# Performance work log

Hardware: AMD Instinct MI355X
Metric: run time of the kernel (lower is better)

Reference implementation:

```python
import jax, jax.numpy as jnp
import numpy as np

N_NODES = 50000
N_EDGES = 400000
N_GRAPHS = 256
NUM_TYPES = 200
EMB = 64
HID = 128
HEADS = 4
GDIM = 256  # graph_embed_dim
NUM_CLASSES = 20
EPS = 1e-5
NEG_SLOPE = 0.2


def _gat_conv(h, src, dst, W, a_src, a_dst, bias, heads, out_c, concat):
    """PyG GATConv (with self-loops already appended to src/dst)."""
    n = h.shape[0]
    x = (h @ W.T).reshape(n, heads, out_c)                       # [N,H,C]
    al_s = jnp.einsum('nhc,hc->nh', x, a_src)                    # [N,H]
    al_d = jnp.einsum('nhc,hc->nh', x, a_dst)
    e = jax.nn.leaky_relu(al_s[src] + al_d[dst], NEG_SLOPE)      # [E',H]
    # segment softmax over destination node
    e_max = jax.ops.segment_max(e, dst, num_segments=n)
    e_exp = jnp.exp(e - e_max[dst])
    denom = jax.ops.segment_sum(e_exp, dst, num_segments=n)
    alpha = e_exp / denom[dst]                                   # [E',H]
    out = jax.ops.segment_sum(alpha[:, :, None] * x[src], dst, num_segments=n)  # [N,H,C]
    out = out.reshape(n, heads * out_c) if concat else out.mean(axis=1)
    return out + bias


def _batchnorm(h, gamma, beta):
    # training-mode BatchNorm1d over node dim (biased variance, as torch)
    m = h.mean(axis=0)
    v = jnp.mean((h - m) ** 2, axis=0)
    return (h - m) * jax.lax.rsqrt(v + EPS) * gamma + beta


def setup_inputs() -> dict:
    key = jax.random.key(0)
    ks = jax.random.split(key, 32)
    s = 0.1
    inp = {
        'x': jax.random.randint(ks[0], (N_NODES,), 0, NUM_TYPES),
        'edge_index': jax.random.randint(ks[1], (2, N_EDGES), 0, N_NODES),
        'depth': jax.random.uniform(ks[2], (N_NODES,), jnp.float32),
        'batch': jnp.sort(jax.random.randint(ks[3], (N_NODES,), 0, N_GRAPHS)),
        'emb_table': jax.random.normal(ks[4], (NUM_TYPES, EMB), jnp.float32) * s,
        'depth_w': jax.random.normal(ks[5], (EMB, 1), jnp.float32) * s,
        'depth_b': jnp.zeros((EMB,), jnp.float32),
        'W0': jax.random.normal(ks[6], (HEADS * HID, EMB), jnp.float32) * s,
        'as0': jax.random.normal(ks[7], (HEADS, HID), jnp.float32) * s,
        'ad0': jax.random.normal(ks[8], (HEADS, HID), jnp.float32) * s,
        'b0': jnp.zeros((HEADS * HID,), jnp.float32),
        'g0': jnp.ones((HEADS * HID,), jnp.float32),
        'be0': jnp.zeros((HEADS * HID,), jnp.float32),
        'W1': jax.random.normal(ks[9], (HEADS * HID, HEADS * HID), jnp.float32) * s,
        'as1': jax.random.normal(ks[10], (HEADS, HID), jnp.float32) * s,
        'ad1': jax.random.normal(ks[11], (HEADS, HID), jnp.float32) * s,
        'b1': jnp.zeros((HEADS * HID,), jnp.float32),
        'g1': jnp.ones((HEADS * HID,), jnp.float32),
        'be1': jnp.zeros((HEADS * HID,), jnp.float32),
        # layer 2: 512 -> 128, 1 head, no concat
        'W2': jax.random.normal(ks[12], (GDIM // 2, HEADS * HID), jnp.float32) * s,
        'as2': jax.random.normal(ks[13], (1, GDIM // 2), jnp.float32) * s,
        'ad2': jax.random.normal(ks[14], (1, GDIM // 2), jnp.float32) * s,
        'b2': jnp.zeros((GDIM // 2,), jnp.float32),
        'g2': jnp.ones((GDIM // 2,), jnp.float32),
        'be2': jnp.zeros((GDIM // 2,), jnp.float32),
        # classifier: 256 -> 256 -> 20
        'cw1': jax.random.normal(ks[15], (GDIM, 2 * (GDIM // 2)), jnp.float32) * s,
        'cb1': jnp.zeros((GDIM,), jnp.float32),
        'cw2': jax.random.normal(ks[16], (NUM_CLASSES, GDIM), jnp.float32) * s,
        'cb2': jnp.zeros((NUM_CLASSES,), jnp.float32),
    }
    return inp


def reference(x, edge_index, depth, batch, emb_table, depth_w, depth_b,
              W0, as0, ad0, b0, g0, be0,
              W1, as1, ad1, b1, g1, be1,
              W2, as2, ad2, b2, g2, be2,
              cw1, cb1, cw2, cb2):
    n = x.shape[0]
    # node features: type embedding + depth projection
    h = emb_table[x] + (depth[:, None] @ depth_w.T + depth_b)    # [N,64]
    # add self-loops once (PyG GATConv default add_self_loops=True)
    loop = jnp.arange(n)
    src = jnp.concatenate([edge_index[0], loop])
    dst = jnp.concatenate([edge_index[1], loop])
    layers = [
        (W0, as0, ad0, b0, g0, be0, HEADS, HID, True),
        (W1, as1, ad1, b1, g1, be1, HEADS, HID, True),
        (W2, as2, ad2, b2, g2, be2, 1, GDIM // 2, False),
    ]
    for (W, a_s, a_d, b, g, be, heads, out_c, concat) in layers:
        h = _gat_conv(h, src, dst, W, a_s, a_d, b, heads, out_c, concat)
        h = _batchnorm(h, g, be)
        h = jax.nn.elu(h)
        # dropout: eval mode -> identity
    # global mean / max pooling per graph
    ones = jnp.ones((n,), h.dtype)
    counts = jax.ops.segment_sum(ones, batch, num_segments=N_GRAPHS)
    h_mean = jax.ops.segment_sum(h, batch, num_segments=N_GRAPHS) / jnp.maximum(counts, 1.0)[:, None]
    h_max = jax.ops.segment_max(h, batch, num_segments=N_GRAPHS)
    emb = jnp.concatenate([h_mean, h_max], axis=-1)              # [G,256]
    # classifier (dropout off in eval)
    hidden = jax.nn.relu(emb @ cw1.T + cb1)
    return hidden @ cw2.T + cb2                                  # [G,20]
```

## Files before the change

kernel.cpp:

```cpp
#include <hip/hip_runtime.h>
#include <hip/hip_bf16.h>

#define N_NODES 50000
#define N_PAD 50048
#define NBY 391
#define N_EDGES 400000
#define EP (N_EDGES + N_NODES)
#define N_GRAPHS 256
#define EMB 64
#define HID 128
#define HEADS 4
#define GDIM 256
#define NUM_CLASSES 20
#define EPS_BN 1e-5f
#define NEG_SLOPE 0.2f
#define NB_AGG 2048

typedef __attribute__((ext_vector_type(8))) short short8;
typedef __attribute__((ext_vector_type(4))) float f32x4;
typedef _Float16 h8 __attribute__((ext_vector_type(8)));
typedef _Float16 h2 __attribute__((ext_vector_type(2)));

#define GLD(g, l)                                                              \
    __builtin_amdgcn_global_load_lds(                                          \
        (const __attribute__((address_space(1))) void*)(g),                    \
        (__attribute__((address_space(3))) void*)(l), 16, 0, 0)

__device__ __forceinline__ unsigned short f2b(float x) {
    union { float f; unsigned u; } a; a.f = x;
    unsigned r = a.u + 0x7FFF + ((a.u >> 16) & 1);
    return (unsigned short)(r >> 16);
}
__device__ __forceinline__ float b2f(unsigned short h) {
    union { unsigned u; float f; } a; a.u = (unsigned)h << 16;
    return a.f;
}

__global__ void k_node_init(const int* __restrict__ x, const float* __restrict__ depth,
                            const float* __restrict__ emb_table, const float* __restrict__ dw,
                            const float* __restrict__ db, float* __restrict__ h) {
    int i = blockIdx.x * blockDim.x + threadIdx.x;
    if (i >= N_NODES * EMB) return;
    int n = i >> 6, c = i & 63;
    h[i] = emb_table[x[n] * EMB + c] + depth[n] * dw[c] + db[c];
}

__global__ void k_deg(const int* __restrict__ ei, int* __restrict__ deg) {
    int e = blockIdx.x * blockDim.x + threadIdx.x;
    if (e >= EP) return;
    int dst = (e < N_EDGES) ? ei[N_EDGES + e] : (e - N_EDGES);
    atomicAdd(&deg[dst], 1);
}

__global__ void k_scanA(const int* __restrict__ deg, int* __restrict__ incl, int* __restrict__ bsums) {
    __shared__ int sh[1024];
    int t = threadIdx.x;
    int i = blockIdx.x * 1024 + t;
    int v = (i < N_NODES) ? deg[i] : 0;
    int xv = v;
    sh[t] = xv;
    __syncthreads();
    for (int off = 1; off < 1024; off <<= 1) {
        int y = (t >= off) ? sh[t - off] : 0;
        __syncthreads();
        xv += y;
        sh[t] = xv;
        __syncthreads();
    }
    if (i < N_NODES) incl[i] = xv;
    if (t == 1023) bsums[blockIdx.x] = xv;
}

__global__ void k_scanC(const int* __restrict__ incl, const int* __restrict__ deg,
                        const int* __restrict__ bsums, int* __restrict__ offs) {
    int i = blockIdx.x * blockDim.x + threadIdx.x;
    int b = i >> 10;
    int add = 0;
    for (int k = 0; k < b; k++) add += bsums[k];
    if (i < N_NODES) offs[i] = incl[i] - deg[i] + add;
    if (i == 0) offs[N_NODES] = EP;
}

__global__ void k_scatter(const int* __restrict__ ei, const int* __restrict__ offs,
                          int* __restrict__ cnt, int* __restrict__ csr) {
    int e = blockIdx.x * blockDim.x + threadIdx.x;
    if (e >= EP) return;
    int src, dst;
    if (e < N_EDGES) { src = ei[e]; dst = ei[N_EDGES + e]; }
    else { src = e - N_EDGES; dst = src; }
    int pos = atomicAdd(&cnt[dst], 1);
    csr[offs[dst] + pos] = src;
}

__device__ __forceinline__ void split1(const float* __restrict__ in, unsigned short* __restrict__ hi,
                                       unsigned short* __restrict__ lo, int i) {
    int f = i * 4;
    float4 v = *(const float4*)(in + f);
    ushort4 h, l;
    h.x = f2b(v.x); l.x = f2b(v.x - b2f(h.x));
    h.y = f2b(v.y); l.y = f2b(v.y - b2f(h.y));
    h.z = f2b(v.z); l.z = f2b(v.z - b2f(h.z));
    h.w = f2b(v.w); l.w = f2b(v.w - b2f(h.w));
    *(ushort4*)(hi + f) = h;
    *(ushort4*)(lo + f) = l;
}

__global__ __launch_bounds__(256) void k_setup(const float* __restrict__ W0, const float* __restrict__ as0,
                                               const float* __restrict__ ad0, const float* __restrict__ W1,
                                               const float* __restrict__ W2,
                                               unsigned short* __restrict__ W0h, unsigned short* __restrict__ W0l,
                                               unsigned short* __restrict__ W1h, unsigned short* __restrict__ W1l,
                                               unsigned short* __restrict__ W2h, unsigned short* __restrict__ W2l,
                                               float* __restrict__ wtil,
                                               float* __restrict__ bn0, float* __restrict__ bn1,
                                               float* __restrict__ bn2) {
    int b = blockIdx.x, t = threadIdx.x;
    if (b < 256) {
        split1(W1, W1h, W1l, b * 256 + t);
    } else if (b < 288) {
        split1(W0, W0h, W0l, (b - 256) * 256 + t);
    } else if (b < 352) {
        split1(W2, W2h, W2l, (b - 288) * 256 + t);
    } else if (b == 352) {
        int h = t >> 6, k = t & 63;
        float ss = 0.f, sd = 0.f;
        for (int c = 0; c < 128; c++) {
            float w = W0[(size_t)(h * 128 + c) * 64 + k];
            ss += w * as0[h * 128 + c];
            sd += w * ad0[h * 128 + c];
        }
        wtil[t] = ss;
        wtil[256 + t] = sd;
    } else {
        for (int i = t; i < 1024; i += 256) { bn0[i] = 0.f; bn1[i] = 0.f; bn2[i] = 0.f; }
    }
}

__global__ __launch_bounds__(256) void k_bnsplit(unsigned short* __restrict__ hi,
                                                 unsigned short* __restrict__ lo,
                                                 const float* __restrict__ sums,
                                                 const float* __restrict__ gamma,
                                                 const float* __restrict__ beta,
                                                 int M, int total4) {
    int i = blockIdx.x * blockDim.x + threadIdx.x;
    if (i >= total4) return;
    int f = i * 4;
    int c = f & (M - 1);
    float4 s4 = *(const float4*)(sums + c);
    float4 q4 = *(const float4*)(sums + M + c);
    float4 g4 = *(const float4*)(gamma + c);
    float4 be4 = *(const float4*)(beta + c);
    const float invN = 1.f / (float)N_NODES;
    float4 sc, sh;
    {
        float m = s4.x * invN; float var = q4.x * invN - m * m;
        sc.x = g4.x * __frsqrt_rn(var + EPS_BN); sh.x = be4.x - m * sc.x;
        m = s4.y * invN; var = q4.y * invN - m * m;
        sc.y = g4.y * __frsqrt_rn(var + EPS_BN); sh.y = be4.y - m * sc.y;
        m = s4.z * invN; var = q4.z * invN - m * m;
        sc.z = g4.z * __frsqrt_rn(var + EPS_BN); sh.z = be4.z - m * sc.z;
        m = s4.w * invN; var = q4.w * invN - m * m;
        sc.w = g4.w * __frsqrt_rn(var + EPS_BN); sh.w = be4.w - m * sc.w;
    }
    ushort4 h4 = *(const ushort4*)(hi + f);
    ushort4 l4 = *(const ushort4*)(lo + f);
    float4 v;
    v.x = b2f(h4.x) + b2f(l4.x);
    v.y = b2f(h4.y) + b2f(l4.y);
    v.z = b2f(h4.z) + b2f(l4.z);
    v.w = b2f(h4.w) + b2f(l4.w);
    float x;
    x = v.x * sc.x + sh.x; v.x = x > 0.f ? x : expm1f(x);
    x = v.y * sc.y + sh.y; v.y = x > 0.f ? x : expm1f(x);
    x = v.z * sc.z + sh.z; v.z = x > 0.f ? x : expm1f(x);
    x = v.w * sc.w + sh.w; v.w = x > 0.f ? x : expm1f(x);
    ushort4 h, l;
    h.x = f2b(v.x); l.x = f2b(v.x - b2f(h.x));
    h.y = f2b(v.y); l.y = f2b(v.y - b2f(h.y));
    h.z = f2b(v.z); l.z = f2b(v.z - b2f(h.z));
    h.w = f2b(v.w); l.w = f2b(v.w - b2f(h.w));
    *(ushort4*)(hi + f) = h;
    *(ushort4*)(lo + f) = l;
}

__global__ __launch_bounds__(256) void k_al0(const float* __restrict__ h0,
                                             const float* __restrict__ wtil,
                                             float* __restrict__ als, float* __restrict__ ald) {
    int wid = threadIdx.x >> 6, lane = threadIdx.x & 63;
    int n = blockIdx.x * 4 + wid;
    if (n >= N_NODES) return;
    float v = h0[(size_t)n * 64 + lane];
#pragma unroll
    for (int h = 0; h < 4; h++) {
        float ps = v * wtil[h * 64 + lane];
        float pd = v * wtil[256 + h * 64 + lane];
        for (int off = 32; off; off >>= 1) {
            ps += __shfl_xor(ps, off);
            pd += __shfl_xor(pd, off);
        }
        if (lane == 0) { als[n * 4 + h] = ps; ald[n * 4 + h] = pd; }
    }
}

__global__ __launch_bounds__(256) void k_agg0(const float* __restrict__ h0,
                                              const float* __restrict__ als,
                                              const float* __restrict__ ald_g,
                                              const int* __restrict__ offs,
                                              const int* __restrict__ csr,
                                              unsigned short* __restrict__ outh,
                                              unsigned short* __restrict__ outl) {
    const int lane = threadIdx.x & 63;
    const int wwid = threadIdx.x >> 6;
    const int q = lane >> 4, l = lane & 15;
    const int gw = blockIdx.x * 4 + wwid;
    const int stride = gridDim.x * 16;
    for (int n = gw * 4 + q; n < N_NODES; n += stride) {
        int s0 = offs[n], s1 = offs[n + 1];
        float aldl = (l < 4) ? ald_g[n * 4 + l] : 0.f;
        float acc[4][4] = {};
        float den[4] = {};
        int e = s0;
        for (; e + 2 <= s1; e += 2) {
            int srcA = csr[e], srcB = csr[e + 1];
            float wA = 0.f, wB = 0.f;
            if (l < 4) {
                float a1 = als[srcA * 4 + l] + aldl;
                a1 = a1 > 0.f ? a1 : NEG_SLOPE * a1;
                wA = expf(a1);
                float a2 = als[srcB * 4 + l] + aldl;
                a2 = a2 > 0.f ? a2 : NEG_SLOPE * a2;
                wB = expf(a2);
            }
            float4 vA = *(const float4*)(h0 + (size_t)srcA * 64 + l * 4);
            float4 vB = *(const float4*)(h0 + (size_t)srcB * 64 + l * 4);
#pragma unroll
            for (int h = 0; h < 4; h++) {
                float whA = __shfl(wA, q * 16 + h);
                float whB = __shfl(wB, q * 16 + h);
                den[h] += whA + whB;
                acc[h][0] += whA * vA.x + whB * vB.x;
                acc[h][1] += whA * vA.y + whB * vB.y;
                acc[h][2] += whA * vA.z + whB * vB.z;
                acc[h][3] += whA * vA.w + whB * vB.w;
            }
        }
        for (; e < s1; e++) {
            int src = csr[e];
            float w = 0.f;
            if (l < 4) {
                float a1 = als[src * 4 + l] + aldl;
                a1 = a1 > 0.f ? a1 : NEG_SLOPE * a1;
                w = expf(a1);
            }
            float4 v = *(const float4*)(h0 + (size_t)src * 64 + l * 4);
#pragma unroll
            for (int h = 0; h < 4; h++) {
                float wh = __shfl(w, q * 16 + h);
                den[h] += wh;
                acc[h][0] += wh * v.x;
                acc[h][1] += wh * v.y;
                acc[h][2] += wh * v.z;
                acc[h][3] += wh * v.w;
            }
        }
#pragma unroll
        for (int h = 0; h < 4; h++) {
            float id = 1.f / den[h];
            float o0 = acc[h][0] * id, o1 = acc[h][1] * id;
            float o2 = acc[h][2] * id, o3 = acc[h][3] * id;
            ushort4 hh, ll;
            hh.x = f2b(o0); ll.x = f2b(o0 - b2f(hh.x));
            hh.y = f2b(o1); ll.y = f2b(o1 - b2f(hh.y));
            hh.z = f2b(o2); ll.z = f2b(o2 - b2f(hh.z));
            hh.w = f2b(o3); ll.w = f2b(o3 - b2f(hh.w));
            size_t idx = (size_t)n * 256 + h * 64 + l * 4;
            *(ushort4*)(outh + idx) = hh;
            *(ushort4*)(outl + idx) = ll;
        }
    }
}

__global__ __launch_bounds__(256) void k_gemm0h(const unsigned short* __restrict__ Ahh,
                                                const unsigned short* __restrict__ Ahl,
                                                const unsigned short* __restrict__ Wh,
                                                const unsigned short* __restrict__ Wl,
                                                const float* __restrict__ bias,
                                                unsigned short* __restrict__ outh,
                                                unsigned short* __restrict__ outl,
                                                float* __restrict__ bnacc) {
    __shared__ short8 sAh[512], sAl[512], sWh[512], sWl[512];
    const int nbx = gridDim.x;
    const int d = blockIdx.y * nbx + blockIdx.x;
    const int by = (d / (8 * nbx)) * 8 + (d & 7);
    const int bx = (d >> 3) % nbx;
    if (by >= NBY) return;
    const int hd = bx;
    const int t = threadIdx.x;
    const int lane = t & 63;
    const int wid = t >> 6;
    const int wm = wid >> 1, wn = wid & 1;
    const int r0 = by * 128;
    const int l15 = lane & 15, quad = lane >> 4;
    f32x4 acc[4][4] = {};
    for (int kb = 0; kb < 64; kb += 32) {
#pragma unroll
        for (int r = 0; r < 2; r++) {
            int c = r * 256 + t;
            int row = c >> 2, q = c & 3;
            size_t gA = ((size_t)(r0 + row) * 256 + hd * 64 + kb) * 2 + q * 16;
            size_t gW = ((size_t)(hd * 128 + row) * 64 + kb) * 2 + q * 16;
            GLD((const char*)Ahh + gA, (char*)sAh + c * 16);
            GLD((const char*)Ahl + gA, (char*)sAl + c * 16);
            GLD((const char*)Wh + gW, (char*)sWh + c * 16);
            GLD((const char*)Wl + gW, (char*)sWl + c * 16);
        }
        __syncthreads();
        short8 a_h[4], a_l[4], w_h[4], w_l[4];
#pragma unroll
        for (int i = 0; i < 4; i++) {
            int ra = (wm * 64 + i * 16 + l15) * 4 + quad;
            int rw = (wn * 64 + i * 16 + l15) * 4 + quad;
            a_h[i] = sAh[ra]; a_l[i] = sAl[ra];
            w_h[i] = sWh[rw]; w_l[i] = sWl[rw];
        }
#pragma unroll
        for (int i = 0; i < 4; i++)
#pragma unroll
            for (int j = 0; j < 4; j++) {
                acc[i][j] = __builtin_amdgcn_mfma_f32_16x16x32_bf16(a_h[i], w_h[j], acc[i][j], 0, 0, 0);
                acc[i][j] = __builtin_amdgcn_mfma_f32_16x16x32_bf16(a_h[i], w_l[j], acc[i][j], 0, 0, 0);
                acc[i][j] = __builtin_amdgcn_mfma_f32_16x16x32_bf16(a_l[i], w_h[j], acc[i][j], 0, 0, 0);
            }
        __syncthreads();
    }
    float colsum[4] = {}, colsq[4] = {};
#pragma unroll
    for (int i = 0; i < 4; i++) {
        int gr = r0 + wm * 64 + i * 16 + quad * 4;
#pragma unroll
        for (int j = 0; j < 4; j++) {
            int gc = hd * 128 + wn * 64 + j * 16 + l15;
            float bv = bias[gc];
#pragma unroll
            for (int rg = 0; rg < 4; rg++) {
                int rr = gr + rg;
                if (rr < N_NODES) {
                    float o = acc[i][j][rg] + bv;
                    unsigned short hh = f2b(o);
                    size_t idx = (size_t)rr * 512 + gc;
                    outh[idx] = hh;
                    outl[idx] = f2b(o - b2f(hh));
                    colsum[j] += o;
                    colsq[j] += o * o;
                }
            }
        }
    }
#pragma unroll
    for (int j = 0; j < 4; j++) {
        colsum[j] += __shfl_xor(colsum[j], 16);
        colsum[j] += __shfl_xor(colsum[j], 32);
        colsq[j] += __shfl_xor(colsq[j], 16);
        colsq[j] += __shfl_xor(colsq[j], 32);
    }
    float* sS = (float*)sAh;
    float* sQ = (float*)sAl;
    __syncthreads();
    if (quad == 0) {
#pragma unroll
        for (int j = 0; j < 4; j++) {
            int c = wn * 64 + j * 16 + l15;
            sS[c * 2 + wm] = colsum[j];
            sQ[c * 2 + wm] = colsq[j];
        }
    }
    __syncthreads();
    if (t < 128) {
        atomicAdd(bnacc + hd * 128 + t, sS[t * 2] + sS[t * 2 + 1]);
        atomicAdd(bnacc + 512 + hd * 128 + t, sQ[t * 2] + sQ[t * 2 + 1]);
    }
}

__global__ __launch_bounds__(256) void k_gemm_mfma(const unsigned short* __restrict__ Ah,
                                                   const unsigned short* __restrict__ Al,
                                                   const unsigned short* __restrict__ Wh,
                                                   const unsigned short* __restrict__ Wl,
                                                   const float* __restrict__ a_src,
                                                   const float* __restrict__ a_dst,
                                                   float* __restrict__ als_g,
                                                   float* __restrict__ ald_g,
                                                   _Float16* __restrict__ out,
                                                   int K, int M, int heads) {
    __shared__ short8 sAh[512], sAl[512], sWh[512], sWl[512];
    const int nbx = gridDim.x;
    const int d = blockIdx.y * nbx + blockIdx.x;
    const int by = (d / (8 * nbx)) * 8 + (d & 7);
    const int bx = (d >> 3) % nbx;
    if (by >= NBY) return;
    const int t = threadIdx.x;
    const int lane = t & 63;
    const int wid = t >> 6;
    const int wm = wid >> 1, wn = wid & 1;
    const int r0 = by * 128, c0 = bx * 128;
    const int l15 = lane & 15, quad = lane >> 4;
    f32x4 acc[4][4] = {};
    for (int kb = 0; kb < K; kb += 32) {
#pragma unroll
        for (int r = 0; r < 2; r++) {
            int c = r * 256 + t;
            int row = c >> 2, q = c & 3;
            size_t gA = ((size_t)(r0 + row) * K + kb) * 2 + q * 16;
            size_t gW = ((size_t)(c0 + row) * K + kb) * 2 + q * 16;
            GLD((const char*)Ah + gA, (char*)sAh + c * 16);
            GLD((const char*)Al + gA, (char*)sAl + c * 16);
            GLD((const char*)Wh + gW, (char*)sWh + c * 16);
            GLD((const char*)Wl + gW, (char*)sWl + c * 16);
        }
        __syncthreads();
        short8 a_h[4], a_l[4], w_h[4], w_l[4];
#pragma unroll
        for (int i = 0; i < 4; i++) {
            int ra = (wm * 64 + i * 16 + l15) * 4 + quad;
            int rw = (wn * 64 + i * 16 + l15) * 4 + quad;
            a_h[i] = sAh[ra]; a_l[i] = sAl[ra];
            w_h[i] = sWh[rw]; w_l[i] = sWl[rw];
        }
#pragma unroll
        for (int i = 0; i < 4; i++)
#pragma unroll
            for (int j = 0; j < 4; j++) {
                acc[i][j] = __builtin_amdgcn_mfma_f32_16x16x32_bf16(a_h[i], w_h[j], acc[i][j], 0, 0, 0);
                acc[i][j] = __builtin_amdgcn_mfma_f32_16x16x32_bf16(a_h[i], w_l[j], acc[i][j], 0, 0, 0);
                acc[i][j] = __builtin_amdgcn_mfma_f32_16x16x32_bf16(a_l[i], w_h[j], acc[i][j], 0, 0, 0);
            }
        __syncthreads();
    }
#pragma unroll
    for (int i = 0; i < 4; i++) {
        int gr = r0 + wm * 64 + i * 16 + quad * 4;
#pragma unroll
        for (int j = 0; j < 4; j++) {
            int gc = c0 + wn * 64 + j * 16 + l15;
#pragma unroll
            for (int rg = 0; rg < 4; rg++) {
                int rr = gr + rg;
                if (rr < N_NODES) out[(size_t)rr * M + gc] = (_Float16)acc[i][j][rg];
            }
        }
    }
    const int hd = bx;
    float ps[4][4] = {}, pd[4][4] = {};
#pragma unroll
    for (int j = 0; j < 4; j++) {
        int ch = wn * 64 + j * 16 + l15;
        float av = a_src[hd * 128 + ch];
        float dv = a_dst[hd * 128 + ch];
#pragma unroll
        for (int i = 0; i < 4; i++)
#pragma unroll
            for (int rg = 0; rg < 4; rg++) {
                ps[i][rg] += acc[i][j][rg] * av;
                pd[i][rg] += acc[i][j][rg] * dv;
            }
    }
#pragma unroll
    for (int m = 1; m < 16; m <<= 1)
#pragma unroll
        for (int i = 0; i < 4; i++)
#pragma unroll
            for (int rg = 0; rg < 4; rg++) {
                ps[i][rg] += __shfl_xor(ps[i][rg], m);
                pd[i][rg] += __shfl_xor(pd[i][rg], m);
            }
    float* sS = (float*)sAh;
    float* sD = (float*)sAl;
    if (l15 == 0) {
#pragma unroll
        for (int i = 0; i < 4; i++)
#pragma unroll
            for (int rg = 0; rg < 4; rg++) {
                int ri = wm * 64 + i * 16 + quad * 4 + rg;
                sS[ri * 2 + wn] = ps[i][rg];
                sD[ri * 2 + wn] = pd[i][rg];
            }
    }
    __syncthreads();
    if (t < 128) {
        int row = r0 + t;
        if (row < N_NODES) {
            als_g[row * heads + hd] = sS[t * 2] + sS[t * 2 + 1];
            ald_g[row * heads + hd] = sD[t * 2] + sD[t * 2 + 1];
        }
    }
}

__global__ __launch_bounds__(256) void k_agg512(const _Float16* __restrict__ xf,
                                                const float* __restrict__ als,
                                                const float* __restrict__ ald_g,
                                                const int* __restrict__ offs,
                                                const int* __restrict__ csr,
                                                const float* __restrict__ bias,
                                                unsigned short* __restrict__ out_h,
                                                unsigned short* __restrict__ out_l,
                                                float* __restrict__ bnacc) {
    __shared__ float pool[4][1024];
    const int wid = threadIdx.x >> 6, lane = threadIdx.x & 63;
    int* s_src = (int*)&pool[wid][0];
    float* s_w = &pool[wid][64];
    const int gw = blockIdx.x * 4 + wid;
    const int nw = gridDim.x * 4;
    const int hh = lane >> 4;
    const int c0 = lane * 8;
    float bias8[8];
#pragma unroll
    for (int k = 0; k < 8; k++) bias8[k] = bias[c0 + k];
    float bns[8] = {}, bnq[8] = {};
    for (int n = gw; n < N_NODES; n += nw) {
        int s0 = offs[n], s1 = offs[n + 1];
        float4 aldv = *(const float4*)(ald_g + n * 4);
        float a[8] = {};
        float den = 0.f;
        for (int base = s0; base < s1; base += 64) {
            int j = base + lane;
            int srcj = 0;
            float4 alv = make_float4(0.f, 0.f, 0.f, 0.f);
            if (j < s1) {
                srcj = csr[j];
                alv = *(const float4*)(als + srcj * 4);
            }
            float e0 = alv.x + aldv.x; e0 = e0 > 0.f ? e0 : NEG_SLOPE * e0;
            float e1 = alv.y + aldv.y; e1 = e1 > 0.f ? e1 : NEG_SLOPE * e1;
            float e2 = alv.z + aldv.z; e2 = e2 > 0.f ? e2 : NEG_SLOPE * e2;
            float e3 = alv.w + aldv.w; e3 = e3 > 0.f ? e3 : NEG_SLOPE * e3;
            s_src[lane] = srcj;
            s_w[0 * 64 + lane] = expf(e0);
            s_w[1 * 64 + lane] = expf(e1);
            s_w[2 * 64 + lane] = expf(e2);
            s_w[3 * 64 + lane] = expf(e3);
            int cend = min(64, s1 - base);
            int e = 0;
            for (; e + 8 <= cend; e += 8) {
                h8 v[8];
                float w[8];
#pragma unroll
                for (int u = 0; u < 8; u++) {
                    v[u] = *(const h8*)(xf + (size_t)s_src[e + u] * 512 + c0);
                    w[u] = s_w[hh * 64 + e + u];
                }
#pragma unroll
                for (int u = 0; u < 8; u++) {
                    den += w[u];
#pragma unroll
                    for (int k = 0; k < 8; k++) a[k] += w[u] * (float)v[u][k];
                }
            }
            for (; e + 2 <= cend; e += 2) {
                h8 vA = *(const h8*)(xf + (size_t)s_src[e] * 512 + c0);
                h8 vB = *(const h8*)(xf + (size_t)s_src[e + 1] * 512 + c0);
                float wA = s_w[hh * 64 + e], wB = s_w[hh * 64 + e + 1];
                den += wA + wB;
#pragma unroll
                for (int k = 0; k < 8; k++) a[k] += wA * (float)vA[k] + wB * (float)vB[k];
            }
            if (e < cend) {
                h8 v = *(const h8*)(xf + (size_t)s_src[e] * 512 + c0);
                float w = s_w[hh * 64 + e];
                den += w;
#pragma unroll
                for (int k = 0; k < 8; k++) a[k] += w * (float)v[k];
            }
        }
        float id = 1.f / den;
        short8 hv, lv;
#pragma unroll
        for (int k = 0; k < 8; k++) {
            float o = a[k] * id + bias8[k];
            unsigned short oh = f2b(o);
            hv[k] = (short)oh;
            lv[k] = (short)f2b(o - b2f(oh));
            bns[k] += o;
            bnq[k] += o * o;
        }
        size_t idx = (size_t)n * 512 + c0;
        *(short8*)(out_h + idx) = hv;
        *(short8*)(out_l + idx) = lv;
    }
#pragma unroll
    for (int k = 0; k < 8; k++) {
        pool[wid][c0 + k] = bns[k];
        pool[wid][512 + c0 + k] = bnq[k];
    }
    __syncthreads();
    for (int t = threadIdx.x; t < 1024; t += 256)
        atomicAdd(bnacc + t, pool[0][t] + pool[1][t] + pool[2][t] + pool[3][t]);
}

__global__ __launch_bounds__(256) void k_agg128(const _Float16* __restrict__ xf,
                                                const float* __restrict__ als,
                                                const float* __restrict__ ald_g,
                                                const int* __restrict__ offs,
                                                const int* __restrict__ csr,
                                                const float* __restrict__ bias,
                                                float* __restrict__ out_f,
                                                float* __restrict__ bnacc) {
    __shared__ float pool[4][256];
    const int wid = threadIdx.x >> 6, lane = threadIdx.x & 63;
    int* s_src = (int*)&pool[wid][0];
    float* s_w = &pool[wid][64];
    const int gw = blockIdx.x * 4 + wid;
    const int nw = gridDim.x * 4;
    const int c = lane * 2;
    const float2 biasv = *(const float2*)(bias + c);
    float bns0 = 0.f, bns1 = 0.f, bnq0 = 0.f, bnq1 = 0.f;
    for (int n = gw; n < N_NODES; n += nw) {
        int s0 = offs[n], s1 = offs[n + 1];
        float aldv = ald_g[n];
        float ax = 0.f, ay = 0.f, den = 0.f;
        for (int base = s0; base < s1; base += 64) {
            int j = base + lane;
            int srcj = 0;
            float alv = 0.f;
            if (j < s1) { srcj = csr[j]; alv = als[srcj]; }
            float e0 = alv + aldv;
            e0 = e0 > 0.f ? e0 : NEG_SLOPE * e0;
            s_src[lane] = srcj;
            s_w[lane] = expf(e0);
            int cend = min(64, s1 - base);
            int e = 0;
            for (; e + 8 <= cend; e += 8) {
                h2 v[8];
                float w[8];
#pragma unroll
                for (int u = 0; u < 8; u++) {
                    v[u] = *(const h2*)(xf + (size_t)s_src[e + u] * 128 + c);
                    w[u] = s_w[e + u];
                }
#pragma unroll
                for (int u = 0; u < 8; u++) {
                    den += w[u];
                    ax += w[u] * (float)v[u][0];
                    ay += w[u] * (float)v[u][1];
                }
            }
            for (; e < cend; e++) {
                h2 v = *(const h2*)(xf + (size_t)s_src[e] * 128 + c);
                float w = s_w[e];
                den += w;
                ax += w * (float)v[0];
                ay += w * (float)v[1];
            }
        }
        float id = 1.f / den;
        float ox = ax * id + biasv.x;
        float oy = ay * id + biasv.y;
        *(float2*)(out_f + (size_t)n * 128 + c) = make_float2(ox, oy);
        bns0 += ox; bnq0 += ox * ox;
        bns1 += oy; bnq1 += oy * oy;
    }
    pool[wid][c] = bns0; pool[wid][c + 1] = bns1;
    pool[wid][128 + c] = bnq0; pool[wid][128 + c + 1] = bnq1;
    __syncthreads();
    {
        int t = threadIdx.x;
        atomicAdd(bnacc + t, pool[0][t] + pool[1][t] + pool[2][t] + pool[3][t]);
    }
}

__global__ void k_graph_bounds(const int* __restrict__ batch, int* __restrict__ goffs) {
    int n = blockIdx.x * blockDim.x + threadIdx.x;
    if (n >= N_NODES) return;
    int b = batch[n];
    int bp = (n == 0) ? -1 : batch[n - 1];
    for (int g = bp + 1; g <= b; g++) goffs[g] = n;
    if (n == N_NODES - 1) {
        for (int g = b + 1; g <= N_GRAPHS; g++) goffs[g] = N_NODES;
    }
}

__global__ __launch_bounds__(256) void k_poolclassify(const float* __restrict__ C,
                                                      const float* __restrict__ bnsums,
                                                      const float* __restrict__ gamma,
                                                      const float* __restrict__ beta,
                                                      const int* __restrict__ goffs,
                                                      const float* __restrict__ cw1, const float* __restrict__ cb1,
                                                      const float* __restrict__ cw2, const float* __restrict__ cb2,
                                                      float* __restrict__ out) {
    __shared__ float er[256];
    __shared__ float red[256];
    int g = blockIdx.x, t = threadIdx.x;
    int c = t & 127, half = t >> 7;
    const float invN = 1.f / (float)N_NODES;
    float m = bnsums[c] * invN;
    float var = bnsums[128 + c] * invN - m * m;
    float sc = gamma[c] * __frsqrt_rn(var + EPS_BN);
    float sh = beta[c] - m * sc;
    int s = goffs[g], e = goffs[g + 1];
    float sum = 0.f, mx = -INFINITY;
    for (int n = s + half; n < e; n += 2) {
        float x = C[(size_t)n * 128 + c] * sc + sh;
        x = x > 0.f ? x : expm1f(x);
        sum += x;
        mx = fmaxf(mx, x);
    }
    red[t] = sum;
    __syncthreads();
    float sumT = red[c] + red[128 + c];
    __syncthreads();
    red[t] = mx;
    __syncthreads();
    float mxT = fmaxf(red[c], red[128 + c]);
    int cnt = e - s;
    if (half == 0) {
        er[c] = sumT / (float)max(cnt, 1);
        er[128 + c] = mxT;
    }
    __syncthreads();
    float acc = cb1[t];
    for (int k = 0; k < 256; k++) acc += er[k] * cw1[t * 256 + k];
    __syncthreads();
    red[t] = fmaxf(acc, 0.f);
    __syncthreads();
    if (t < NUM_CLASSES) {
        float o = cb2[t];
        for (int k = 0; k < 256; k++) o += red[k] * cw2[t * 256 + k];
        out[g * NUM_CLASSES + t] = o;
    }
}

extern "C" void kernel_launch(void* const* d_in, const int* in_sizes, int n_in,
                              void* d_out, int out_size, void* d_ws, size_t ws_size,
                              hipStream_t stream) {
    (void)in_sizes; (void)n_in; (void)out_size; (void)ws_size;
    const int* x = (const int*)d_in[0];
    const int* ei = (const int*)d_in[1];
    const float* depth = (const float*)d_in[2];
    const int* batch = (const int*)d_in[3];
    const float* emb_table = (const float*)d_in[4];
    const float* depth_w = (const float*)d_in[5];
    const float* depth_b = (const float*)d_in[6];
    const float* W0 = (const float*)d_in[7];
    const float* as0 = (const float*)d_in[8];
    const float* ad0 = (const float*)d_in[9];
    const float* b0 = (const float*)d_in[10];
    const float* g0 = (const float*)d_in[11];
    const float* be0 = (const float*)d_in[12];
    const float* W1 = (const float*)d_in[13];
    const float* as1 = (const float*)d_in[14];
    const float* ad1 = (const float*)d_in[15];
    const float* b1 = (const float*)d_in[16];
    const float* g1 = (const float*)d_in[17];
    const float* be1 = (const float*)d_in[18];
    const float* W2 = (const float*)d_in[19];
    const float* as2 = (const float*)d_in[20];
    const float* ad2 = (const float*)d_in[21];
    const float* b2 = (const float*)d_in[22];
    const float* g2 = (const float*)d_in[23];
    const float* be2 = (const float*)d_in[24];
    const float* cw1 = (const float*)d_in[25];
    const float* cb1 = (const float*)d_in[26];
    const float* cw2 = (const float*)d_in[27];
    const float* cb2 = (const float*)d_in[28];
    float* out = (float*)d_out;

    size_t off = 0;
    char* base = (char*)d_ws;
    auto carve = [&](size_t bytes) -> void* {
        void* p = base + off;
        off += (bytes + 255) & ~(size_t)255;
        return p;
    };
    float* B = (float*)carve((size_t)N_NODES * 64 * 4 + (size_t)N_PAD * 256 * 2 * 2);
    unsigned short* Ah = (unsigned short*)carve((size_t)N_NODES * 512 * 2);
    unsigned short* Al = (unsigned short*)carve((size_t)N_NODES * 512 * 2);
    unsigned short* W0h = (unsigned short*)carve((size_t)512 * 64 * 2);
    unsigned short* W0l = (unsigned short*)carve((size_t)512 * 64 * 2);
    unsigned short* W1h = (unsigned short*)carve((size_t)512 * 512 * 2);
    unsigned short* W1l = (unsigned short*)carve((size_t)512 * 512 * 2);
    unsigned short* W2h = (unsigned short*)carve((size_t)128 * 512 * 2);
    unsigned short* W2l = (unsigned short*)carve((size_t)128 * 512 * 2);
    float* als = (float*)carve((size_t)N_NODES * HEADS * 4);
    float* ald = (float*)carve((size_t)N_NODES * HEADS * 4);
    float* bn0 = (float*)carve(1024 * 4);
    float* bn1 = (float*)carve(1024 * 4);
    float* bn2 = (float*)carve(1024 * 4);
    float* wtil = (float*)carve(512 * 4);
    int* deg = (int*)carve((size_t)2 * N_NODES * 4);
    int* cnt = deg + N_NODES;
    int* incl = (int*)carve((size_t)N_NODES * 4);
    int* offs = (int*)carve((size_t)(N_NODES + 1) * 4);
    int* bsums = (int*)carve(64 * 4);
    int* csr = (int*)carve((size_t)EP * 4);
    int* goffs = (int*)carve((size_t)(N_GRAPHS + 1) * 4);

    float* h0 = B;
    unsigned short* hth = (unsigned short*)((char*)B + (size_t)N_NODES * 64 * 4);
    unsigned short* htl = hth + (size_t)N_PAD * 256;
    _Float16* Bh = (_Float16*)B;
    float* C = (float*)Ah;

    const int TPB = 256;
    int gbN = (N_NODES + TPB - 1) / TPB;
    int gbE = (EP + TPB - 1) / TPB;
    int nbScan = (N_NODES + 1023) / 1024;
    int gbNode4 = (N_NODES + 3) / 4;
    dim3 g512(4, 392);
    dim3 g128(1, 391);

    hipMemsetAsync(deg, 0, (size_t)2 * N_NODES * 4, stream);
    k_setup<<<354, TPB, 0, stream>>>(W0, as0, ad0, W1, W2, W0h, W0l, W1h, W1l, W2h, W2l,
                                     wtil, bn0, bn1, bn2);
    k_deg<<<gbE, TPB, 0, stream>>>(ei, deg);
    k_scanA<<<nbScan, 1024, 0, stream>>>(deg, incl, bsums);
    k_scanC<<<gbN, TPB, 0, stream>>>(incl, deg, bsums, offs);
    k_scatter<<<gbE, TPB, 0, stream>>>(ei, offs, cnt, csr);
    k_graph_bounds<<<gbN, TPB, 0, stream>>>(batch, goffs);

    k_node_init<<<(N_NODES * EMB + TPB - 1) / TPB, TPB, 0, stream>>>(x, depth, emb_table, depth_w, depth_b, h0);
    k_al0<<<gbNode4, TPB, 0, stream>>>(h0, wtil, als, ald);
    k_agg0<<<NB_AGG, TPB, 0, stream>>>(h0, als, ald, offs, csr, hth, htl);
    k_gemm0h<<<g512, TPB, 0, stream>>>(hth, htl, W0h, W0l, b0, Ah, Al, bn0);
    k_bnsplit<<<(N_NODES * 512 / 4 + TPB - 1) / TPB, TPB, 0, stream>>>(Ah, Al, bn0, g0, be0, 512, N_NODES * 512 / 4);
    k_gemm_mfma<<<g512, TPB, 0, stream>>>(Ah, Al, W1h, W1l, as1, ad1, als, ald, Bh, 512, 512, HEADS);
    k_agg512<<<NB_AGG, TPB, 0, stream>>>(Bh, als, ald, offs, csr, b1, Ah, Al, bn1);
    k_bnsplit<<<(N_NODES * 512 / 4 + TPB - 1) / TPB, TPB, 0, stream>>>(Ah, Al, bn1, g1, be1, 512, N_NODES * 512 / 4);
    k_gemm_mfma<<<g128, TPB, 0, stream>>>(Ah, Al, W2h, W2l, as2, ad2, als, ald, Bh, 512, 128, 1);
    k_agg128<<<NB_AGG, TPB, 0, stream>>>(Bh, als, ald, offs, csr, b2, C, bn2);
    k_poolclassify<<<N_GRAPHS, TPB, 0, stream>>>(C, bn2, g2, be2, goffs, cw1, cb1, cw2, cb2, out);
}
```

Measured before the change: 712.1 us.

## Replace split-bf16 hi/lo emulation with single fp16 and double-buffer GEMM staging

Removes the three-pass split-bf16 (hi/lo) scheme that approximated fp32 GEMMs. Activations and weights are now stored as single fp16 arrays and each product uses one fp16 MFMA. This cuts MFMA count threefold and halves activation and weight memory traffic in the GEMM, aggregation and batchnorm kernels. The GEMM loops also gain double-buffered LDS staging so the next k-slice loads overlap compute. The cost is lower precision, since fp16 has fewer mantissa bits than the split pair and a narrower range, which may matter for tolerance.

```diff
diff --git a/kernel.cpp b/kernel.cpp
--- a/kernel.cpp
+++ b/kernel.cpp
@@ -1,5 +1,4 @@
 #include <hip/hip_runtime.h>
-#include <hip/hip_bf16.h>
 
 #define N_NODES 50000
 #define N_PAD 50048
@@ -16,25 +15,15 @@
 #define NEG_SLOPE 0.2f
 #define NB_AGG 2048
 
-typedef __attribute__((ext_vector_type(8))) short short8;
 typedef __attribute__((ext_vector_type(4))) float f32x4;
 typedef _Float16 h8 __attribute__((ext_vector_type(8)));
+typedef _Float16 h4 __attribute__((ext_vector_type(4)));
 typedef _Float16 h2 __attribute__((ext_vector_type(2)));
 
 #define GLD(g, l)                                                              \
     __builtin_amdgcn_global_load_lds(                                          \
         (const __attribute__((address_space(1))) void*)(g),                    \
         (__attribute__((address_space(3))) void*)(l), 16, 0, 0)
-
-__device__ __forceinline__ unsigned short f2b(float x) {
-    union { float f; unsigned u; } a; a.f = x;
-    unsigned r = a.u + 0x7FFF + ((a.u >> 16) & 1);
-    return (unsigned short)(r >> 16);
-}
-__device__ __forceinline__ float b2f(unsigned short h) {
-    union { unsigned u; float f; } a; a.u = (unsigned)h << 16;
-    return a.f;
-}
 
 __global__ void k_node_init(const int* __restrict__ x, const float* __restrict__ depth,
                             const float* __restrict__ emb_table, const float* __restrict__ dw,
@@ -92,35 +81,29 @@
     csr[offs[dst] + pos] = src;
 }
 
-__device__ __forceinline__ void split1(const float* __restrict__ in, unsigned short* __restrict__ hi,
-                                       unsigned short* __restrict__ lo, int i) {
+__device__ __forceinline__ void cvt1(const float* __restrict__ in, _Float16* __restrict__ o, int i) {
     int f = i * 4;
     float4 v = *(const float4*)(in + f);
-    ushort4 h, l;
-    h.x = f2b(v.x); l.x = f2b(v.x - b2f(h.x));
-    h.y = f2b(v.y); l.y = f2b(v.y - b2f(h.y));
-    h.z = f2b(v.z); l.z = f2b(v.z - b2f(h.z));
-    h.w = f2b(v.w); l.w = f2b(v.w - b2f(h.w));
-    *(ushort4*)(hi + f) = h;
-    *(ushort4*)(lo + f) = l;
+    h4 r;
+    r[0] = (_Float16)v.x; r[1] = (_Float16)v.y; r[2] = (_Float16)v.z; r[3] = (_Float16)v.w;
+    *(h4*)(o + f) = r;
 }
 
 __global__ __launch_bounds__(256) void k_setup(const float* __restrict__ W0, const float* __restrict__ as0,
                                                const float* __restrict__ ad0, const float* __restrict__ W1,
                                                const float* __restrict__ W2,
-                                               unsigned short* __restrict__ W0h, unsigned short* __restrict__ W0l,
-                                               unsigned short* __restrict__ W1h, unsigned short* __restrict__ W1l,
-                                               unsigned short* __restrict__ W2h, unsigned short* __restrict__ W2l,
+                                               _Float16* __restrict__ W0f, _Float16* __restrict__ W1f,
+                                               _Float16* __restrict__ W2f,
                                                float* __restrict__ wtil,
                                                float* __restrict__ bn0, float* __restrict__ bn1,
                                                float* __restrict__ bn2) {
     int b = blockIdx.x, t = threadIdx.x;
     if (b < 256) {
-        split1(W1, W1h, W1l, b * 256 + t);
+        cvt1(W1, W1f, b * 256 + t);
     } else if (b < 288) {
-        split1(W0, W0h, W0l, (b - 256) * 256 + t);
+        cvt1(W0, W0f, (b - 256) * 256 + t);
     } else if (b < 352) {
-        split1(W2, W2h, W2l, (b - 288) * 256 + t);
+        cvt1(W2, W2f, (b - 288) * 256 + t);
     } else if (b == 352) {
         int h = t >> 6, k = t & 63;
         float ss = 0.f, sd = 0.f;
@@ -136,51 +119,29 @@
     }
 }
 
-__global__ __launch_bounds__(256) void k_bnsplit(unsigned short* __restrict__ hi,
-                                                 unsigned short* __restrict__ lo,
-                                                 const float* __restrict__ sums,
-                                                 const float* __restrict__ gamma,
-                                                 const float* __restrict__ beta,
-                                                 int M, int total4) {
+__global__ __launch_bounds__(256) void k_bnelu(_Float16* __restrict__ a,
+                                               const float* __restrict__ sums,
+                                               const float* __restrict__ gamma,
+                                               const float* __restrict__ beta,
+                                               int M, int total8) {
     int i = blockIdx.x * blockDim.x + threadIdx.x;
-    if (i >= total4) return;
-    int f = i * 4;
-    int c = f & (M - 1);
-    float4 s4 = *(const float4*)(sums + c);
-    float4 q4 = *(const float4*)(sums + M + c);
-    float4 g4 = *(const float4*)(gamma + c);
-    float4 be4 = *(const float4*)(beta + c);
+    if (i >= total8) return;
+    size_t f = (size_t)i * 8;
+    int c = (int)(f & (size_t)(M - 1));
+    h8 v = *(h8*)(a + f);
     const float invN = 1.f / (float)N_NODES;
-    float4 sc, sh;
-    {
-        float m = s4.x * invN; float var = q4.x * invN - m * m;
-        sc.x = g4.x * __frsqrt_rn(var + EPS_BN); sh.x = be4.x - m * sc.x;
-        m = s4.y * invN; var = q4.y * invN - m * m;
-        sc.y = g4.y * __frsqrt_rn(var + EPS_BN); sh.y = be4.y - m * sc.y;
-        m = s4.z * invN; var = q4.z * invN - m * m;
-        sc.z = g4.z * __frsqrt_rn(var + EPS_BN); sh.z = be4.z - m * sc.z;
-        m = s4.w * invN; var = q4.w * invN - m * m;
-        sc.w = g4.w * __frsqrt_rn(var + EPS_BN); sh.w = be4.w - m * sc.w;
-    }
-    ushort4 h4 = *(const ushort4*)(hi + f);
-    ushort4 l4 = *(const ushort4*)(lo + f);
-    float4 v;
-    v.x = b2f(h4.x) + b2f(l4.x);
-    v.y = b2f(h4.y) + b2f(l4.y);
-    v.z = b2f(h4.z) + b2f(l4.z);
-    v.w = b2f(h4.w) + b2f(l4.w);
-    float x;
-    x = v.x * sc.x + sh.x; v.x = x > 0.f ? x : expm1f(x);
-    x = v.y * sc.y + sh.y; v.y = x > 0.f ? x : expm1f(x);
-    x = v.z * sc.z + sh.z; v.z = x > 0.f ? x : expm1f(x);
-    x = v.w * sc.w + sh.w; v.w = x > 0.f ? x : expm1f(x);
-    ushort4 h, l;
-    h.x = f2b(v.x); l.x = f2b(v.x - b2f(h.x));
-    h.y = f2b(v.y); l.y = f2b(v.y - b2f(h.y));
-    h.z = f2b(v.z); l.z = f2b(v.z - b2f(h.z));
-    h.w = f2b(v.w); l.w = f2b(v.w - b2f(h.w));
-    *(ushort4*)(hi + f) = h;
-    *(ushort4*)(lo + f) = l;
+    h8 o;
+#pragma unroll
+    for (int k = 0; k < 8; k++) {
+        float m = sums[c + k] * invN;
+        float var = sums[M + c + k] * invN - m * m;
+        float sc = gamma[c + k] * __frsqrt_rn(var + EPS_BN);
+        float sh = beta[c + k] - m * sc;
+        float x = (float)v[k] * sc + sh;
+        x = x > 0.f ? x : expm1f(x);
+        o[k] = (_Float16)x;
+    }
+    *(h8*)(a + f) = o;
 }
 
 __global__ __launch_bounds__(256) void k_al0(const float* __restrict__ h0,
@@ -207,8 +168,7 @@
                                               const float* __restrict__ ald_g,
                                               const int* __restrict__ offs,
                                               const int* __restrict__ csr,
-                                              unsigned short* __restrict__ outh,
-                                              unsigned short* __restrict__ outl) {
+                                              _Float16* __restrict__ outh) {
     const int lane = threadIdx.x & 63;
     const int wwid = threadIdx.x >> 6;
     const int q = lane >> 4, l = lane & 15;
@@ -266,29 +226,22 @@
 #pragma unroll
         for (int h = 0; h < 4; h++) {
             float id = 1.f / den[h];
-            float o0 = acc[h][0] * id, o1 = acc[h][1] * id;
-            float o2 = acc[h][2] * id, o3 = acc[h][3] * id;
-            ushort4 hh, ll;
-            hh.x = f2b(o0); ll.x = f2b(o0 - b2f(hh.x));
-            hh.y = f2b(o1); ll.y = f2b(o1 - b2f(hh.y));
-            hh.z = f2b(o2); ll.z = f2b(o2 - b2f(hh.z));
-            hh.w = f2b(o3); ll.w = f2b(o3 - b2f(hh.w));
-            size_t idx = (size_t)n * 256 + h * 64 + l * 4;
-            *(ushort4*)(outh + idx) = hh;
-            *(ushort4*)(outl + idx) = ll;
-        }
-    }
-}
-
-__global__ __launch_bounds__(256) void k_gemm0h(const unsigned short* __restrict__ Ahh,
-                                                const unsigned short* __restrict__ Ahl,
-                                                const unsigned short* __restrict__ Wh,
-                                                const unsigned short* __restrict__ Wl,
+            h4 hv;
+            hv[0] = (_Float16)(acc[h][0] * id);
+            hv[1] = (_Float16)(acc[h][1] * id);
+            hv[2] = (_Float16)(acc[h][2] * id);
+            hv[3] = (_Float16)(acc[h][3] * id);
+            *(h4*)(outh + (size_t)n * 256 + h * 64 + l * 4) = hv;
+        }
+    }
+}
+
+__global__ __launch_bounds__(256) void k_gemm0h(const _Float16* __restrict__ A,
+                                                const _Float16* __restrict__ W,
                                                 const float* __restrict__ bias,
-                                                unsigned short* __restrict__ outh,
-                                                unsigned short* __restrict__ outl,
+                                                _Float16* __restrict__ outA,
                                                 float* __restrict__ bnacc) {
-    __shared__ short8 sAh[512], sAl[512], sWh[512], sWl[512];
+    __shared__ h8 sA[2][512], sW[2][512];
     const int nbx = gridDim.x;
     const int d = blockIdx.y * nbx + blockIdx.x;
     const int by = (d / (8 * nbx)) * 8 + (d & 7);
@@ -302,35 +255,34 @@
     const int r0 = by * 128;
     const int l15 = lane & 15, quad = lane >> 4;
     f32x4 acc[4][4] = {};
-    for (int kb = 0; kb < 64; kb += 32) {
+    auto stage = [&](int buf, int kb) {
 #pragma unroll
         for (int r = 0; r < 2; r++) {
             int c = r * 256 + t;
             int row = c >> 2, q = c & 3;
             size_t gA = ((size_t)(r0 + row) * 256 + hd * 64 + kb) * 2 + q * 16;
             size_t gW = ((size_t)(hd * 128 + row) * 64 + kb) * 2 + q * 16;
-            GLD((const char*)Ahh + gA, (char*)sAh + c * 16);
-            GLD((const char*)Ahl + gA, (char*)sAl + c * 16);
-            GLD((const char*)Wh + gW, (char*)sWh + c * 16);
-            GLD((const char*)Wl + gW, (char*)sWl + c * 16);
-        }
-        __syncthreads();
-        short8 a_h[4], a_l[4], w_h[4], w_l[4];
+            GLD((const char*)A + gA, (char*)&sA[buf][0] + c * 16);
+            GLD((const char*)W + gW, (char*)&sW[buf][0] + c * 16);
+        }
+    };
+    stage(0, 0);
+    __syncthreads();
+#pragma unroll
+    for (int ki = 0; ki < 2; ki++) {
+        int cur = ki & 1;
+        if (ki + 1 < 2) stage(cur ^ 1, (ki + 1) * 32);
+        h8 a[4], w[4];
 #pragma unroll
         for (int i = 0; i < 4; i++) {
-            int ra = (wm * 64 + i * 16 + l15) * 4 + quad;
-            int rw = (wn * 64 + i * 16 + l15) * 4 + quad;
-            a_h[i] = sAh[ra]; a_l[i] = sAl[ra];
-            w_h[i] = sWh[rw]; w_l[i] = sWl[rw];
+            a[i] = sA[cur][(wm * 64 + i * 16 + l15) * 4 + quad];
+            w[i] = sW[cur][(wn * 64 + i * 16 + l15) * 4 + quad];
         }
 #pragma unroll
         for (int i = 0; i < 4; i++)
 #pragma unroll
-            for (int j = 0; j < 4; j++) {
-                acc[i][j] = __builtin_amdgcn_mfma_f32_16x16x32_bf16(a_h[i], w_h[j], acc[i][j], 0, 0, 0);
-                acc[i][j] = __builtin_amdgcn_mfma_f32_16x16x32_bf16(a_h[i], w_l[j], acc[i][j], 0, 0, 0);
-                acc[i][j] = __builtin_amdgcn_mfma_f32_16x16x32_bf16(a_l[i], w_h[j], acc[i][j], 0, 0, 0);
-            }
+            for (int j = 0; j < 4; j++)
+                acc[i][j] = __builtin_amdgcn_mfma_f32_16x16x32_f16(a[i], w[j], acc[i][j], 0, 0, 0);
         __syncthreads();
     }
     float colsum[4] = {}, colsq[4] = {};
@@ -346,10 +298,7 @@
                 int rr = gr + rg;
                 if (rr < N_NODES) {
                     float o = acc[i][j][rg] + bv;
-                    unsigned short hh = f2b(o);
-                    size_t idx = (size_t)rr * 512 + gc;
-                    outh[idx] = hh;
-                    outl[idx] = f2b(o - b2f(hh));
+                    outA[(size_t)rr * 512 + gc] = (_Float16)o;
                     colsum[j] += o;
                     colsq[j] += o * o;
                 }
@@ -363,8 +312,8 @@
         colsq[j] += __shfl_xor(colsq[j], 16);
         colsq[j] += __shfl_xor(colsq[j], 32);
     }
-    float* sS = (float*)sAh;
-    float* sQ = (float*)sAl;
+    float* sS = (float*)&sA[0][0];
+    float* sQ = (float*)&sW[0][0];
     __syncthreads();
     if (quad == 0) {
 #pragma unroll
@@ -381,17 +330,15 @@
     }
 }
 
-__global__ __launch_bounds__(256) void k_gemm_mfma(const unsigned short* __restrict__ Ah,
-                                                   const unsigned short* __restrict__ Al,
-                                                   const unsigned short* __restrict__ Wh,
-                                                   const unsigned short* __restrict__ Wl,
+__global__ __launch_bounds__(256) void k_gemm_mfma(const _Float16* __restrict__ A,
+                                                   const _Float16* __restrict__ W,
                                                    const float* __restrict__ a_src,
                                                    const float* __restrict__ a_dst,
                                                    float* __restrict__ als_g,
                                                    float* __restrict__ ald_g,
                                                    _Float16* __restrict__ out,
                                                    int K, int M, int heads) {
-    __shared__ short8 sAh[512], sAl[512], sWh[512], sWl[512];
+    __shared__ h8 sA[2][512], sW[2][512];
     const int nbx = gridDim.x;
     const int d = blockIdx.y * nbx + blockIdx.x;
     const int by = (d / (8 * nbx)) * 8 + (d & 7);
@@ -404,35 +351,34 @@
     const int r0 = by * 128, c0 = bx * 128;
     const int l15 = lane & 15, quad = lane >> 4;
     f32x4 acc[4][4] = {};
-    for (int kb = 0; kb < K; kb += 32) {
+    auto stage = [&](int buf, int kb) {
 #pragma unroll
         for (int r = 0; r < 2; r++) {
             int c = r * 256 + t;
             int row = c >> 2, q = c & 3;
             size_t gA = ((size_t)(r0 + row) * K + kb) * 2 + q * 16;
             size_t gW = ((size_t)(c0 + row) * K + kb) * 2 + q * 16;
-            GLD((const char*)Ah + gA, (char*)sAh + c * 16);
-            GLD((const char*)Al + gA, (char*)sAl + c * 16);
-            GLD((const char*)Wh + gW, (char*)sWh + c * 16);
-            GLD((const char*)Wl + gW, (char*)sWl + c * 16);
-        }
-        __syncthreads();
-        short8 a_h[4], a_l[4], w_h[4], w_l[4];
+            GLD((const char*)A + gA, (char*)&sA[buf][0] + c * 16);
+            GLD((const char*)W + gW, (char*)&sW[buf][0] + c * 16);
+        }
+    };
+    stage(0, 0);
+    __syncthreads();
+    const int nkb = K >> 5;
+    for (int ki = 0; ki < nkb; ki++) {
+        int cur = ki & 1;
+        if (ki + 1 < nkb) stage(cur ^ 1, (ki + 1) * 32);
+        h8 a[4], w[4];
 #pragma unroll
         for (int i = 0; i < 4; i++) {
-            int ra = (wm * 64 + i * 16 + l15) * 4 + quad;
-            int rw = (wn * 64 + i * 16 + l15) * 4 + quad;
-            a_h[i] = sAh[ra]; a_l[i] = sAl[ra];
-            w_h[i] = sWh[rw]; w_l[i] = sWl[rw];
+            a[i] = sA[cur][(wm * 64 + i * 16 + l15) * 4 + quad];
+            w[i] = sW[cur][(wn * 64 + i * 16 + l15) * 4 + quad];
         }
 #pragma unroll
         for (int i = 0; i < 4; i++)
 #pragma unroll
-            for (int j = 0; j < 4; j++) {
-                acc[i][j] = __builtin_amdgcn_mfma_f32_16x16x32_bf16(a_h[i], w_h[j], acc[i][j], 0, 0, 0);
-                acc[i][j] = __builtin_amdgcn_mfma_f32_16x16x32_bf16(a_h[i], w_l[j], acc[i][j], 0, 0, 0);
-                acc[i][j] = __builtin_amdgcn_mfma_f32_16x16x32_bf16(a_l[i], w_h[j], acc[i][j], 0, 0, 0);
-            }
+            for (int j = 0; j < 4; j++)
+                acc[i][j] = __builtin_amdgcn_mfma_f32_16x16x32_f16(a[i], w[j], acc[i][j], 0, 0, 0);
         __syncthreads();
     }
 #pragma unroll
@@ -472,8 +418,8 @@
                 ps[i][rg] += __shfl_xor(ps[i][rg], m);
                 pd[i][rg] += __shfl_xor(pd[i][rg], m);
             }
-    float* sS = (float*)sAh;
-    float* sD = (float*)sAl;
+    float* sS = (float*)&sA[0][0];
+    float* sD = (float*)&sW[0][0];
     if (l15 == 0) {
 #pragma unroll
         for (int i = 0; i < 4; i++)
@@ -500,8 +446,7 @@
                                                 const int* __restrict__ offs,
                                                 const int* __restrict__ csr,
                                                 const float* __restrict__ bias,
-                                                unsigned short* __restrict__ out_h,
-                                                unsigned short* __restrict__ out_l,
+                                                _Float16* __restrict__ out16,
                                                 float* __restrict__ bnacc) {
     __shared__ float pool[4][1024];
     const int wid = threadIdx.x >> 6, lane = threadIdx.x & 63;
@@ -571,19 +516,15 @@
             }
         }
         float id = 1.f / den;
-        short8 hv, lv;
+        h8 ov;
 #pragma unroll
         for (int k = 0; k < 8; k++) {
             float o = a[k] * id + bias8[k];
-            unsigned short oh = f2b(o);
-            hv[k] = (short)oh;
-            lv[k] = (short)f2b(o - b2f(oh));
+            ov[k] = (_Float16)o;
             bns[k] += o;
             bnq[k] += o * o;
         }
-        size_t idx = (size_t)n * 512 + c0;
-        *(short8*)(out_h + idx) = hv;
-        *(short8*)(out_l + idx) = lv;
+        *(h8*)(out16 + (size_t)n * 512 + c0) = ov;
     }
 #pragma unroll
     for (int k = 0; k < 8; k++) {
@@ -769,15 +710,11 @@
         off += (bytes + 255) & ~(size_t)255;
         return p;
     };
-    float* B = (float*)carve((size_t)N_NODES * 64 * 4 + (size_t)N_PAD * 256 * 2 * 2);
-    unsigned short* Ah = (unsigned short*)carve((size_t)N_NODES * 512 * 2);
-    unsigned short* Al = (unsigned short*)carve((size_t)N_NODES * 512 * 2);
-    unsigned short* W0h = (unsigned short*)carve((size_t)512 * 64 * 2);
-    unsigned short* W0l = (unsigned short*)carve((size_t)512 * 64 * 2);
-    unsigned short* W1h = (unsigned short*)carve((size_t)512 * 512 * 2);
-    unsigned short* W1l = (unsigned short*)carve((size_t)512 * 512 * 2);
-    unsigned short* W2h = (unsigned short*)carve((size_t)128 * 512 * 2);
-    unsigned short* W2l = (unsigned short*)carve((size_t)128 * 512 * 2);
+    float* B = (float*)carve((size_t)N_NODES * 512 * 2);
+    _Float16* A16 = (_Float16*)carve((size_t)N_PAD * 512 * 2);
+    _Float16* W0f = (_Float16*)carve((size_t)512 * 64 * 2);
+    _Float16* W1f = (_Float16*)carve((size_t)512 * 512 * 2);
+    _Float16* W2f = (_Float16*)carve((size_t)128 * 512 * 2);
     float* als = (float*)carve((size_t)N_NODES * HEADS * 4);
     float* ald = (float*)carve((size_t)N_NODES * HEADS * 4);
     float* bn0 = (float*)carve(1024 * 4);
@@ -793,10 +730,9 @@
     int* goffs = (int*)carve((size_t)(N_GRAPHS + 1) * 4);
 
     float* h0 = B;
-    unsigned short* hth = (unsigned short*)((char*)B + (size_t)N_NODES * 64 * 4);
-    unsigned short* htl = hth + (size_t)N_PAD * 256;
+    _Float16* hth = (_Float16*)((char*)B + (size_t)N_NODES * 64 * 4);
     _Float16* Bh = (_Float16*)B;
-    float* C = (float*)Ah;
+    float* C = (float*)A16;
 
     const int TPB = 256;
     int gbN = (N_NODES + TPB - 1) / TPB;
@@ -807,8 +743,7 @@
     dim3 g128(1, 391);
 
     hipMemsetAsync(deg, 0, (size_t)2 * N_NODES * 4, stream);
-    k_setup<<<354, TPB, 0, stream>>>(W0, as0, ad0, W1, W2, W0h, W0l, W1h, W1l, W2h, W2l,
-                                     wtil, bn0, bn1, bn2);
+    k_setup<<<354, TPB, 0, stream>>>(W0, as0, ad0, W1, W2, W0f, W1f, W2f, wtil, bn0, bn1, bn2);
     k_deg<<<gbE, TPB, 0, stream>>>(ei, deg);
     k_scanA<<<nbScan, 1024, 0, stream>>>(deg, incl, bsums);
     k_scanC<<<gbN, TPB, 0, stream>>>(incl, deg, bsums, offs);
@@ -817,13 +752,13 @@
 
     k_node_init<<<(N_NODES * EMB + TPB - 1) / TPB, TPB, 0, stream>>>(x, depth, emb_table, depth_w, depth_b, h0);
     k_al0<<<gbNode4, TPB, 0, stream>>>(h0, wtil, als, ald);
-    k_agg0<<<NB_AGG, TPB, 0, stream>>>(h0, als, ald, offs, csr, hth, htl);
-    k_gemm0h<<<g512, TPB, 0, stream>>>(hth, htl, W0h, W0l, b0, Ah, Al, bn0);
-    k_bnsplit<<<(N_NODES * 512 / 4 + TPB - 1) / TPB, TPB, 0, stream>>>(Ah, Al, bn0, g0, be0, 512, N_NODES * 512 / 4);
-    k_gemm_mfma<<<g512, TPB, 0, stream>>>(Ah, Al, W1h, W1l, as1, ad1, als, ald, Bh, 512, 512, HEADS);
-    k_agg512<<<NB_AGG, TPB, 0, stream>>>(Bh, als, ald, offs, csr, b1, Ah, Al, bn1);
-    k_bnsplit<<<(N_NODES * 512 / 4 + TPB - 1) / TPB, TPB, 0, stream>>>(Ah, Al, bn1, g1, be1, 512, N_NODES * 512 / 4);
-    k_gemm_mfma<<<g128, TPB, 0, stream>>>(Ah, Al, W2h, W2l, as2, ad2, als, ald, Bh, 512, 128, 1);
+    k_agg0<<<NB_AGG, TPB, 0, stream>>>(h0, als, ald, offs, csr, hth);
+    k_gemm0h<<<g512, TPB, 0, stream>>>(hth, W0f, b0, A16, bn0);
+    k_bnelu<<<(N_NODES * 512 / 8 + TPB - 1) / TPB, TPB, 0, stream>>>(A16, bn0, g0, be0, 512, N_NODES * 512 / 8);
+    k_gemm_mfma<<<g512, TPB, 0, stream>>>(A16, W1f, as1, ad1, als, ald, Bh, 512, 512, HEADS);
+    k_agg512<<<NB_AGG, TPB, 0, stream>>>(Bh, als, ald, offs, csr, b1, A16, bn1);
+    k_bnelu<<<(N_NODES * 512 / 8 + TPB - 1) / TPB, TPB, 0, stream>>>(A16, bn1, g1, be1, 512, N_NODES * 512 / 8);
+    k_gemm_mfma<<<g128, TPB, 0, stream>>>(A16, W2f, as2, ad2, als, ald, Bh, 512, 128, 1);
     k_agg128<<<NB_AGG, TPB, 0, stream>>>(Bh, als, ald, offs, csr, b2, C, bn2);
     k_poolclassify<<<N_GRAPHS, TPB, 0, stream>>>(C, bn2, g2, be2, goffs, cw1, cb1, cw2, cb2, out);
 }
```

After: 910.4 us. 27.8% more time.
